# Optimization experiments

Measured on AMD Instinct MI355X. Metric: run time of the kernel, lower is better.

Reference implementation:

```python
import math
import jax, jax.numpy as jnp
import numpy as np

B, L, H = 32, 1024, 128

def setup_inputs() -> dict:
    key = jax.random.key(0)
    k1, k2, k3, k4 = jax.random.split(key, 4)
    a = jax.random.normal(k1, (B, L, H), dtype=jnp.float32)
    b = jax.random.normal(k2, (B, L, H), dtype=jnp.float32)
    mask_a = jax.random.randint(k3, (B, L, 1), 0, 2, dtype=jnp.int32)
    mask_b = jax.random.randint(k4, (B, L, 1), 0, 2, dtype=jnp.int32)
    temperature = jnp.asarray(1.0 / math.sqrt(H), dtype=jnp.float32)
    return {"a": a, "b": b, "mask_a": mask_a, "mask_b": mask_b, "temperature": temperature}

def reference(a, b, mask_a, mask_b, temperature):
    # scores: [B, La, Lb]
    scores = jnp.einsum('bld,bmd->blm', a, b) * temperature
    # outer product of token validity masks -> pair mask [B, La, Lb]
    mask = jnp.einsum('blk,bmk->blm', mask_a.astype(jnp.float32), mask_b.astype(jnp.float32)) > 0
    scores = jnp.where(mask, scores, jnp.float32(-10000.0))
    attention_a = jax.nn.softmax(scores, axis=1)  # normalize over La (columns)
    attention_b = jax.nn.softmax(scores, axis=2)  # normalize over Lb (rows)
    feature_a = jnp.einsum('blm,bmd->bld', attention_b, b)
    feature_b = jnp.einsum('blm,bmd->bld', attention_a, a)  # valid since La == Lb
    return (feature_a, feature_b)
```

## Files before the change

kernel.cpp:

```cpp
#include <hip/hip_runtime.h>
#include <math.h>

#define BN 32
#define LL 1024
#define HH 128

typedef __attribute__((ext_vector_type(8))) short short8;
typedef __attribute__((ext_vector_type(4))) float f32x4;

static const size_t SZ_BF = (size_t)BN * LL * HH * 2;

__device__ __forceinline__ ushort f2bf(float x) {
  union { float f; unsigned u; } c; c.f = x;
  unsigned r = c.u + 0x7fffu + ((c.u >> 16) & 1u);
  return (ushort)(r >> 16);
}
__device__ __forceinline__ float bf2f(ushort h) {
  union { unsigned u; float f; } c; c.u = ((unsigned)h) << 16;
  return c.f;
}
__device__ __forceinline__ short8 ld8(const ushort* p) {
  return *(const short8*)p;
}

__device__ __forceinline__ size_t chunkS(int bb, int g, int k) {
  return (((size_t)bb * 64 + g) * 4 + k) * 512;
}
__device__ __forceinline__ size_t chunkT(int bb, int dg, int mb) {
  return (((size_t)bb * 8 + dg) * 32 + mb) * 512;
}

__global__ __launch_bounds__(256) void k_convert(
    const float* __restrict__ a, const float* __restrict__ b,
    const int* __restrict__ mask_b,
    ushort* __restrict__ abfs, ushort* __restrict__ bbfs,
    ushort* __restrict__ aTs, ushort* __restrict__ bTs,
    float* __restrict__ meanb, float* __restrict__ invmean) {
  int bb = blockIdx.y;
  int l0 = blockIdx.x * 64;
  int which = blockIdx.z;
  const float* src = which ? b : a;
  ushort* dstS = which ? bbfs : abfs;
  ushort* dstT = which ? bTs : aTs;
  float* dmean = which ? meanb : invmean;
  __shared__ __align__(16) ushort T[128][72];
  __shared__ float accS[128];
  __shared__ float wgt[64];
  int t = threadIdx.x;
  if (t < 128) accS[t] = 0.f;
  if (t < 64)
    wgt[t] = which ? 1.0f : ((mask_b[bb * LL + l0 + t] == 0) ? 1.0f : 0.0f);
  int lrow = t >> 5;
  int dcol = (t & 31) * 4;
#pragma unroll
  for (int p = 0; p < 8; ++p) {
    int l = p * 8 + lrow;
    float4 v = *(const float4*)&src[((size_t)bb * LL + l0 + l) * HH + dcol];
    ushort4 u;
    u.x = f2bf(v.x); u.y = f2bf(v.y); u.z = f2bf(v.z); u.w = f2bf(v.w);
    int g = (l0 >> 4) + (l >> 4);
    int k = dcol >> 5, quadc = (dcol >> 3) & 3, j = dcol & 7;
    *(ushort4*)&dstS[chunkS(bb, g, k) + (size_t)(quadc * 16 + (l & 15)) * 8 + j] = u;
    T[dcol + 0][l] = u.x; T[dcol + 1][l] = u.y;
    T[dcol + 2][l] = u.z; T[dcol + 3][l] = u.w;
  }
  __syncthreads();
#pragma unroll
  for (int c = 0; c < 4; ++c) {
    int cid = c * 4 + (t >> 6);
    int dg = cid >> 1, mloc = cid & 1;
    int lane = t & 63, l16c = lane & 15, qc = lane >> 4;
    int row = dg * 16 + l16c, colb = mloc * 32 + qc * 8;
    uint2 vlo = *(const uint2*)&T[row][colb];
    uint2 vhi = *(const uint2*)&T[row][colb + 4];
    union { uint4 u4; short8 s8; ushort us[8]; } cv_;
    cv_.u4 = make_uint4(vlo.x, vlo.y, vhi.x, vhi.y);
    *(short8*)&dstT[chunkT(bb, dg, (l0 >> 5) + mloc) + (size_t)lane * 8] = cv_.s8;
    float s = 0.f;
#pragma unroll
    for (int jj = 0; jj < 8; ++jj) s += wgt[colb + jj] * bf2f(cv_.us[jj]);
    atomicAdd(&accS[row], s);
  }
  __syncthreads();
  if (t < 128) atomicAdd(&dmean[bb * HH + t], accS[t]);
}


__global__ __launch_bounds__(256, 2) void k_colsum(
    const ushort* __restrict__ abfs, const ushort* __restrict__ bbfs,
    ushort* __restrict__ aTm,
    const int* __restrict__ mask_a, const int* __restrict__ mask_b,
    const float* __restrict__ temp_p, float2* __restrict__ cc) {
  int wg = blockIdx.x;
  int xcd = wg & 7, k_ = wg >> 3;
  int bb = (k_ >> 4) * 8 + xcd;
  int m0 = (k_ & 15) * 64;
  int t = threadIdx.x;
  int w = t >> 6, lane = t & 63, l16 = lane & 15, quad = lane >> 4;
  float temp = temp_p[0];
  __shared__ __align__(16) float biasA[LL];
  __shared__ float csred[4][4][16];
  __shared__ float invS[64];
  for (int i = t; i < LL; i += 256)
    biasA[i] = mask_a[bb * LL + i] ? 0.0f : -10000.0f;

  short8 Bm[4][4];
  float biasB_mt[4];
#pragma unroll
  for (int mt = 0; mt < 4; ++mt) {
    int m = m0 + mt * 16 + l16;
    biasB_mt[mt] = mask_b[bb * LL + m] ? 0.0f : -10000.0f;
#pragma unroll
    for (int k = 0; k < 4; ++k)
      Bm[mt][k] = ld8(&bbfs[chunkS(bb, (m0 >> 4) + mt, k) + (size_t)lane * 8]);
  }
  __syncthreads();

  float cs[4] = {0.f, 0.f, 0.f, 0.f};
  short8 Al0[4], Al1[4];

#define LOADAL(AlX, IT)                                                       \
  {                                                                           \
    _Pragma("unroll") for (int k = 0; k < 4; ++k)                             \
        AlX[k] = ld8(&abfs[chunkS(bb, w * 16 + (IT), k) + (size_t)lane * 8]); \
  }

#define CSCOMPUTE(AlX, IT)                                                    \
  {                                                                           \
    int lbase = w * 256 + (IT) * 16;                                          \
    f32x4 bA = *(const f32x4*)&biasA[lbase + quad * 4];                       \
    _Pragma("unroll") for (int mt = 0; mt < 4; ++mt) {                        \
      f32x4 sacc = {0.f, 0.f, 0.f, 0.f};                                      \
      _Pragma("unroll") for (int k = 0; k < 4; ++k)                           \
          sacc = __builtin_amdgcn_mfma_f32_16x16x32_bf16(AlX[k], Bm[mt][k],   \
                                                         sacc, 0, 0, 0);      \
      _Pragma("unroll") for (int r = 0; r < 4; ++r)                           \
          cs[mt] += __expf(sacc[r] * temp + bA[r] + biasB_mt[mt]);            \
    }                                                                         \
  }

  LOADAL(Al0, 0);
  for (int it = 0; it < 16; it += 2) {
    LOADAL(Al1, it + 1);
    CSCOMPUTE(Al0, it);
    LOADAL(Al0, (it + 2) & 15);
    CSCOMPUTE(Al1, it + 1);
  }
#undef LOADAL
#undef CSCOMPUTE

#pragma unroll
  for (int mt = 0; mt < 4; ++mt) {
    cs[mt] += __shfl_xor(cs[mt], 16);
    cs[mt] += __shfl_xor(cs[mt], 32);
  }
  if (lane < 16) {
#pragma unroll
    for (int mt = 0; mt < 4; ++mt) csred[w][mt][l16] = cs[mt];
  }
  __syncthreads();
  if (t < 64) {
    int mt = t >> 4, ml = t & 15;
    float s = csred[0][mt][ml] + csred[1][mt][ml] + csred[2][mt][ml] + csred[3][mt][ml];
    int m = m0 + t;
    float bB = mask_b[bb * LL + m] ? 0.0f : -10000.0f;
    float inv = s > 0.f ? 1.0f / s : 0.0f;
    invS[t] = inv;
    cc[bb * LL + m] = make_float2(inv, bB);
  }
  __syncthreads();

#pragma unroll
  for (int q = 0; q < 4; ++q) {
    int cid = q * 4 + (t >> 6);
    int dg = cid >> 1, mloc = cid & 1;
    int ln = t & 63;
    ushort* ap = &aTm[chunkT(bb, dg, (m0 >> 5) + mloc) + (size_t)ln * 8];
    short8 v = ld8(ap);
    int mb = mloc * 32 + (ln >> 4) * 8;
    ushort o[8];
#pragma unroll
    for (int j = 0; j < 8; ++j) o[j] = f2bf(bf2f((ushort)v[j]) * invS[mb + j]);
    *(short8*)ap = *(short8*)&o[0];
  }
}

__global__ __launch_bounds__(256, 2) void k_features(
    const ushort* __restrict__ abfs, const ushort* __restrict__ bbfs,
    const ushort* __restrict__ aTs, const ushort* __restrict__ bTs,
    const int* __restrict__ mask_a, const float* __restrict__ temp_p,
    const float2* __restrict__ cc, const float* __restrict__ meanb,
    const float* __restrict__ invmean, float* __restrict__ out) {
  int wg = blockIdx.x;
  int xcd = wg & 7, k_ = wg >> 3;
  int bb = (k_ >> 4) * 8 + xcd;
  int l0 = (k_ & 15) * 64;
  int t = threadIdx.x;
  int w = t >> 6, lane = t & 63, l16 = lane & 15, quad = lane >> 4;
  float temp = temp_p[0];

  __shared__ float2 ccs[LL];
  __shared__ __align__(16) ushort Pa[2][64 * 72];
  __shared__ float rspart[4][64];
  __shared__ float rsfin[64];

  for (int i = t; i < LL; i += 256) ccs[i] = cc[bb * LL + i];

  float biasA_lt[4];
  short8 Afix[4][4];
#pragma unroll
  for (int lt = 0; lt < 4; ++lt) {
    int l = l0 + lt * 16 + l16;
    biasA_lt[lt] = mask_a[bb * LL + l] ? 0.0f : -10000.0f;
#pragma unroll
    for (int k = 0; k < 4; ++k)
      Afix[lt][k] = ld8(&abfs[chunkS(bb, (l0 >> 4) + lt, k) + (size_t)lane * 8]);
  }

  f32x4 accA[4][2], accB[4][2];
  f32x4 zero = {0.f, 0.f, 0.f, 0.f};
#pragma unroll
  for (int lt = 0; lt < 4; ++lt)
#pragma unroll
    for (int dt = 0; dt < 2; ++dt) { accA[lt][dt] = zero; accB[lt][dt] = zero; }
  float rs_lt[4] = {0.f, 0.f, 0.f, 0.f};
  __syncthreads();

  short8 Am0[4], Am1[4];
  float cv0[4], cv1[4];
  short8 Bb0[2][2], Ba0[2][2], Bb1[2][2], Ba1[2][2];

#define LOADAM(AmX, cvX, M0)                                                  \
  {                                                                           \
    _Pragma("unroll") for (int k = 0; k < 4; ++k)                             \
        AmX[k] = ld8(&bbfs[chunkS(bb, ((M0) >> 4) + w, k) + (size_t)lane * 8]); \
    _Pragma("unroll") for (int r = 0; r < 4; ++r)                             \
        cvX[r] = ccs[(M0) + w * 16 + quad * 4 + r].y;                         \
  }

#define LOADBT(BbX, BaX, M0)                                                  \
  {                                                                           \
    _Pragma("unroll") for (int dt = 0; dt < 2; ++dt) {                        \
      _Pragma("unroll") for (int ks = 0; ks < 2; ++ks) {                      \
        size_t cb = chunkT(bb, w * 2 + dt, ((M0) >> 5) + ks) + (size_t)lane * 8; \
        BbX[dt][ks] = ld8(&bTs[cb]);                                          \
        BaX[dt][ks] = ld8(&aTs[cb]);                                          \
      }                                                                       \
    }                                                                         \
  }

#define SPHASE(AmX, cvX, PBUFI)                                               \
  {                                                                           \
    ushort* pa = &Pa[PBUFI][0];                                               \
    _Pragma("unroll") for (int lt = 0; lt < 4; ++lt) {                        \
      f32x4 sacc = zero;                                                      \
      _Pragma("unroll") for (int k = 0; k < 4; ++k)                           \
          sacc = __builtin_amdgcn_mfma_f32_16x16x32_bf16(AmX[k], Afix[lt][k], \
                                                         sacc, 0, 0, 0);      \
      ushort pav[4];                                                          \
      _Pragma("unroll") for (int r = 0; r < 4; ++r) {                         \
        float e = __expf(sacc[r] * temp + biasA_lt[lt] + cvX[r]);             \
        pav[r] = f2bf(e);                                                     \
        rs_lt[lt] += bf2f(pav[r]);                                            \
      }                                                                       \
      uint2 ka;                                                               \
      ka.x = (uint)pav[0] | ((uint)pav[1] << 16);                             \
      ka.y = (uint)pav[2] | ((uint)pav[3] << 16);                             \
      int pidx = (lt * 16 + l16) * 72 + w * 16 + quad * 4;                    \
      *(uint2*)&pa[pidx] = ka;                                                \
    }                                                                         \
  }

#define FPHASE(PBUFI, BbX, BaX)                                               \
  {                                                                           \
    const ushort* pa = &Pa[PBUFI][0];                                         \
    _Pragma("unroll") for (int lt = 0; lt < 4; ++lt) {                        \
      _Pragma("unroll") for (int ks = 0; ks < 2; ++ks) {                      \
        int ridx = (lt * 16 + l16) * 72 + ks * 32 + quad * 8;                 \
        short8 PaF = *(const short8*)&pa[ridx];                               \
        _Pragma("unroll") for (int dt = 0; dt < 2; ++dt) {                    \
          accA[lt][dt] = __builtin_amdgcn_mfma_f32_16x16x32_bf16(             \
              PaF, BbX[dt][ks], accA[lt][dt], 0, 0, 0);                       \
          accB[lt][dt] = __builtin_amdgcn_mfma_f32_16x16x32_bf16(             \
              PaF, BaX[dt][ks], accB[lt][dt], 0, 0, 0);                       \
        }                                                                     \
      }                                                                       \
    }                                                                         \
  }

  LOADAM(Am0, cv0, 0);
  LOADBT(Bb0, Ba0, 0);
  LOADAM(Am1, cv1, 64);
  SPHASE(Am0, cv0, 0);
  __syncthreads();

  for (int kk = 0; kk < 7; ++kk) {
    int mA = (2 * kk + 1) * 64;
    LOADBT(Bb1, Ba1, mA);
    LOADAM(Am0, cv0, mA + 64);
    SPHASE(Am1, cv1, 1);
    FPHASE(0, Bb0, Ba0);
    __syncthreads();
    LOADBT(Bb0, Ba0, mA + 64);
    LOADAM(Am1, cv1, mA + 128);
    SPHASE(Am0, cv0, 0);
    FPHASE(1, Bb1, Ba1);
    __syncthreads();
  }

  LOADBT(Bb1, Ba1, 960);
  SPHASE(Am1, cv1, 1);
  FPHASE(0, Bb0, Ba0);
  __syncthreads();
  FPHASE(1, Bb1, Ba1);

#undef LOADAM
#undef LOADBT
#undef SPHASE
#undef FPHASE

#pragma unroll
  for (int lt = 0; lt < 4; ++lt) {
    rs_lt[lt] += __shfl_xor(rs_lt[lt], 16);
    rs_lt[lt] += __shfl_xor(rs_lt[lt], 32);
  }
  if (lane < 16) {
#pragma unroll
    for (int lt = 0; lt < 4; ++lt) rspart[w][lt * 16 + l16] = rs_lt[lt];
  }
  __syncthreads();
  if (t < 64)
    rsfin[t] = rspart[0][t] + rspart[1][t] + rspart[2][t] + rspart[3][t];
  __syncthreads();

  float* outA = out;
  float* outB = out + (size_t)BN * LL * HH;
#pragma unroll
  for (int dt = 0; dt < 2; ++dt) {
    int d = w * 32 + dt * 16 + l16;
    float mb = meanb[bb * HH + d] * (1.0f / 1024.0f);
    float im = invmean[bb * HH + d] * (1.0f / 1024.0f);
#pragma unroll
    for (int lt = 0; lt < 4; ++lt) {
#pragma unroll
      for (int r = 0; r < 4; ++r) {
        int l = lt * 16 + quad * 4 + r;
        float rsv = rsfin[l];
        float fa = (rsv > 0.f) ? accA[lt][dt][r] / rsv : mb;
        float fb = accB[lt][dt][r] + im;
        __builtin_nontemporal_store(fa, &outA[((size_t)bb * LL + l0 + l) * HH + d]);
        __builtin_nontemporal_store(fb, &outB[((size_t)bb * LL + l0 + l) * HH + d]);
      }
    }
  }
}

extern "C" void kernel_launch(void* const* d_in, const int* in_sizes, int n_in,
                              void* d_out, int out_size, void* d_ws, size_t ws_size,
                              hipStream_t stream) {
  const float* a = (const float*)d_in[0];
  const float* b = (const float*)d_in[1];
  const int* mask_a = (const int*)d_in[2];
  const int* mask_b = (const int*)d_in[3];
  const float* temp = (const float*)d_in[4];
  float* out = (float*)d_out;

  char* wsb = (char*)d_ws;
  ushort* abfs = (ushort*)(wsb + 0 * SZ_BF);
  ushort* bbfs = (ushort*)(wsb + 1 * SZ_BF);
  ushort* aTs  = (ushort*)(wsb + 2 * SZ_BF);
  ushort* bTs  = (ushort*)(wsb + 3 * SZ_BF);
  float2* cc  = (float2*)(wsb + 4 * SZ_BF);
  float* meanb   = (float*)(wsb + 4 * SZ_BF + (size_t)BN * LL * sizeof(float2));
  float* invmean = meanb + BN * HH;

  hipMemsetAsync(meanb, 0, 2 * BN * HH * sizeof(float), stream);
  k_convert<<<dim3(16, 32, 2), 256, 0, stream>>>(a, b, mask_b, abfs, bbfs, aTs,
                                                 bTs, meanb, invmean);
  k_colsum<<<dim3(512), 256, 0, stream>>>(abfs, bbfs, aTs, mask_a, mask_b, temp, cc);
  k_features<<<dim3(512), 256, 0, stream>>>(abfs, bbfs, aTs, bTs, mask_a, temp,
                                            cc, meanb, invmean, out);
  (void)in_sizes; (void)n_in; (void)out_size; (void)ws_size;
}
```

Before: 167.8 us.

## Materialize exponentiated scores in colsum pass and reuse them in feature GEMM

The column-sum kernel now writes the bf16 exponentiated masked scores to a workspace buffer in a tiled layout. A new feature kernel reads that buffer instead of recomputing the score GEMM and exponentials, and gets the row sums via an MFMA against a ones vector. This removes the duplicated QK^T and exp work but adds a large write and read of the score matrix through memory. The new path only runs when the workspace is large enough; otherwise the old kernels are used.

```diff
diff --git a/kernel.cpp b/kernel.cpp
--- a/kernel.cpp
+++ b/kernel.cpp
@@ -28,6 +28,9 @@
 }
 __device__ __forceinline__ size_t chunkT(int bb, int dg, int mb) {
   return (((size_t)bb * 8 + dg) * 32 + mb) * 512;
+}
+__device__ __forceinline__ size_t chunkE(int bb, int lg, int mk) {
+  return (((size_t)bb * 64 + lg) * 32 + mk) * 512;
 }
 
 __global__ __launch_bounds__(256) void k_convert(
@@ -185,6 +188,196 @@
   }
 }
 
+__global__ __launch_bounds__(256, 2) void k_colsum_e(
+    const ushort* __restrict__ abfs, const ushort* __restrict__ bbfs,
+    ushort* __restrict__ aTm, const int* __restrict__ mask_a,
+    const int* __restrict__ mask_b, const float* __restrict__ temp_p,
+    float2* __restrict__ cc, ushort* __restrict__ Ebuf) {
+  int wg = blockIdx.x;
+  int xcd = wg & 7, k_ = wg >> 3;
+  int bb = (k_ >> 4) * 8 + xcd;
+  int m0 = (k_ & 15) * 64;
+  int t = threadIdx.x;
+  int w = t >> 6, lane = t & 63, l16 = lane & 15, quad = lane >> 4;
+  float temp = temp_p[0];
+  __shared__ __align__(16) float biasA[LL];
+  __shared__ float csred[4][4][16];
+  __shared__ float invS[64];
+  __shared__ __align__(16) ushort Et[4][16][72];
+  for (int i = t; i < LL; i += 256)
+    biasA[i] = mask_a[bb * LL + i] ? 0.0f : -10000.0f;
+
+  short8 Bm[4][4];
+  float biasB_mt[4];
+#pragma unroll
+  for (int mt = 0; mt < 4; ++mt) {
+    int m = m0 + mt * 16 + l16;
+    biasB_mt[mt] = mask_b[bb * LL + m] ? 0.0f : -10000.0f;
+#pragma unroll
+    for (int k = 0; k < 4; ++k)
+      Bm[mt][k] = ld8(&bbfs[chunkS(bb, (m0 >> 4) + mt, k) + (size_t)lane * 8]);
+  }
+  __syncthreads();
+
+  float cs[4] = {0.f, 0.f, 0.f, 0.f};
+  short8 Al0[4], Al1[4];
+
+#define LOADAL(AlX, IT)                                                       \
+  {                                                                           \
+    _Pragma("unroll") for (int k = 0; k < 4; ++k)                             \
+        AlX[k] = ld8(&abfs[chunkS(bb, w * 16 + (IT), k) + (size_t)lane * 8]); \
+  }
+
+#define CSCOMPUTE_E(AlX, IT)                                                  \
+  {                                                                           \
+    f32x4 bA = *(const f32x4*)&biasA[w * 256 + (IT) * 16 + quad * 4];         \
+    _Pragma("unroll") for (int mt = 0; mt < 4; ++mt) {                        \
+      f32x4 sacc = {0.f, 0.f, 0.f, 0.f};                                      \
+      _Pragma("unroll") for (int k = 0; k < 4; ++k)                           \
+          sacc = __builtin_amdgcn_mfma_f32_16x16x32_bf16(AlX[k], Bm[mt][k],   \
+                                                         sacc, 0, 0, 0);      \
+      _Pragma("unroll") for (int r = 0; r < 4; ++r) {                         \
+        float e = __expf(sacc[r] * temp + bA[r] + biasB_mt[mt]);              \
+        cs[mt] += e;                                                          \
+        Et[w][quad * 4 + r][mt * 16 + l16] = f2bf(e);     \
+      }                                                                       \
+    }                                                                         \
+        \
+    _Pragma("unroll") for (int ks = 0; ks < 2; ++ks) {                        \
+      short8 ef = *(const short8*)&Et[w][l16][ks * 32 + quad * 8];            \
+      *(short8*)&Ebuf[chunkE(bb, w * 16 + (IT), (m0 >> 5) + ks) +             \
+                      (size_t)lane * 8] = ef;                                 \
+    }                                                                         \
+  }
+
+  LOADAL(Al0, 0);
+  for (int it = 0; it < 16; it += 2) {
+    LOADAL(Al1, it + 1);
+    CSCOMPUTE_E(Al0, it);
+    LOADAL(Al0, (it + 2) & 15);
+    CSCOMPUTE_E(Al1, it + 1);
+  }
+#undef LOADAL
+#undef CSCOMPUTE_E
+
+#pragma unroll
+  for (int mt = 0; mt < 4; ++mt) {
+    cs[mt] += __shfl_xor(cs[mt], 16);
+    cs[mt] += __shfl_xor(cs[mt], 32);
+  }
+  if (lane < 16) {
+#pragma unroll
+    for (int mt = 0; mt < 4; ++mt) csred[w][mt][l16] = cs[mt];
+  }
+  __syncthreads();
+  if (t < 64) {
+    int mt = t >> 4, ml = t & 15;
+    float s = csred[0][mt][ml] + csred[1][mt][ml] + csred[2][mt][ml] + csred[3][mt][ml];
+    int m = m0 + t;
+    float bB = mask_b[bb * LL + m] ? 0.0f : -10000.0f;
+    float inv = s > 0.f ? 1.0f / s : 0.0f;
+    invS[t] = inv;
+    cc[bb * LL + m] = make_float2(inv, bB);
+  }
+  __syncthreads();
+
+#pragma unroll
+  for (int q = 0; q < 4; ++q) {
+    int cid = q * 4 + (t >> 6);
+    int dg = cid >> 1, mloc = cid & 1;
+    int ln = t & 63;
+    ushort* ap = &aTm[chunkT(bb, dg, (m0 >> 5) + mloc) + (size_t)ln * 8];
+    short8 v = ld8(ap);
+    int mb = mloc * 32 + (ln >> 4) * 8;
+    ushort o[8];
+#pragma unroll
+    for (int j = 0; j < 8; ++j) o[j] = f2bf(bf2f((ushort)v[j]) * invS[mb + j]);
+    *(short8*)ap = *(short8*)&o[0];
+  }
+}
+
+__global__ __launch_bounds__(256, 2) void k_fgemm(
+    const ushort* __restrict__ aTs, const ushort* __restrict__ bTs,
+    const ushort* __restrict__ Ebuf, const float* __restrict__ meanb,
+    const float* __restrict__ invmean, float* __restrict__ out) {
+  int wg = blockIdx.x;
+  int xcd = wg & 7, k_ = wg >> 3;
+  int bb = (k_ >> 4) * 8 + xcd;
+  int l0 = (k_ & 15) * 64;
+  int t = threadIdx.x;
+  int w = t >> 6, lane = t & 63, l16 = lane & 15, quad = lane >> 4;
+
+  f32x4 accA[4][2], accB[4][2], accR[4];
+  f32x4 zero = {0.f, 0.f, 0.f, 0.f};
+#pragma unroll
+  for (int lt = 0; lt < 4; ++lt) {
+    accR[lt] = zero;
+#pragma unroll
+    for (int dt = 0; dt < 2; ++dt) { accA[lt][dt] = zero; accB[lt][dt] = zero; }
+  }
+  short8 ones;
+#pragma unroll
+  for (int j = 0; j < 8; ++j) ones[j] = (short)0x3F80;
+
+  short8 Ef0[4], Ef1[4], Tb0[2], Tb1[2], Ta0[2], Ta1[2];
+
+#define LOADOP(EfX, TbX, TaX, MS)                                             \
+  {                                                                           \
+    _Pragma("unroll") for (int lt = 0; lt < 4; ++lt)                          \
+        EfX[lt] = ld8(&Ebuf[chunkE(bb, (l0 >> 4) + lt, (MS)) + (size_t)lane * 8]); \
+    _Pragma("unroll") for (int dt = 0; dt < 2; ++dt) {                        \
+      size_t cb = chunkT(bb, w * 2 + dt, (MS)) + (size_t)lane * 8;            \
+      TbX[dt] = ld8(&bTs[cb]);                                                \
+      TaX[dt] = ld8(&aTs[cb]);                                                \
+    }                                                                         \
+  }
+
+#define FMAOP(EfX, TbX, TaX)                                                  \
+  {                                                                           \
+    _Pragma("unroll") for (int lt = 0; lt < 4; ++lt) {                        \
+      accR[lt] = __builtin_amdgcn_mfma_f32_16x16x32_bf16(ones, EfX[lt],       \
+                                                         accR[lt], 0, 0, 0); \
+      _Pragma("unroll") for (int dt = 0; dt < 2; ++dt) {                      \
+        accA[lt][dt] = __builtin_amdgcn_mfma_f32_16x16x32_bf16(               \
+            TbX[dt], EfX[lt], accA[lt][dt], 0, 0, 0);                         \
+        accB[lt][dt] = __builtin_amdgcn_mfma_f32_16x16x32_bf16(               \
+            TaX[dt], EfX[lt], accB[lt][dt], 0, 0, 0);                         \
+      }                                                                       \
+    }                                                                         \
+  }
+
+  LOADOP(Ef0, Tb0, Ta0, 0);
+  for (int ms = 0; ms < 32; ms += 2) {
+    LOADOP(Ef1, Tb1, Ta1, ms + 1);
+    FMAOP(Ef0, Tb0, Ta0);
+    LOADOP(Ef0, Tb0, Ta0, (ms + 2) & 31);
+    FMAOP(Ef1, Tb1, Ta1);
+  }
+#undef LOADOP
+#undef FMAOP
+
+  float* outA = out;
+  float* outB = out + (size_t)BN * LL * HH;
+#pragma unroll
+  for (int dt = 0; dt < 2; ++dt) {
+#pragma unroll
+    for (int r = 0; r < 4; ++r) {
+      int d = w * 32 + dt * 16 + quad * 4 + r;
+      float mb = meanb[bb * HH + d] * (1.0f / 1024.0f);
+      float im = invmean[bb * HH + d] * (1.0f / 1024.0f);
+#pragma unroll
+      for (int lt = 0; lt < 4; ++lt) {
+        int l = l0 + lt * 16 + l16;
+        float rsv = accR[lt][r];
+        float fa = (rsv > 0.f) ? accA[lt][dt][r] / rsv : mb;
+        float fb = accB[lt][dt][r] + im;
+        __builtin_nontemporal_store(fa, &outA[((size_t)bb * LL + l) * HH + d]);
+        __builtin_nontemporal_store(fb, &outB[((size_t)bb * LL + l) * HH + d]);
+      }
+    }
+  }
+}
+
 __global__ __launch_bounds__(256, 2) void k_features(
     const ushort* __restrict__ abfs, const ushort* __restrict__ bbfs,
     const ushort* __restrict__ aTs, const ushort* __restrict__ bTs,
@@ -373,12 +566,25 @@
   float2* cc  = (float2*)(wsb + 4 * SZ_BF);
   float* meanb   = (float*)(wsb + 4 * SZ_BF + (size_t)BN * LL * sizeof(float2));
   float* invmean = meanb + BN * HH;
+  size_t e_off = 4 * SZ_BF + (size_t)BN * LL * sizeof(float2) +
+                 2 * (size_t)BN * HH * sizeof(float);
+  e_off = (e_off + 1023) & ~(size_t)1023;
+  ushort* Ebuf = (ushort*)(wsb + e_off);
+  size_t need = e_off + (size_t)BN * LL * LL * 2;
+  bool use_e = (ws_size >= need);
 
   hipMemsetAsync(meanb, 0, 2 * BN * HH * sizeof(float), stream);
   k_convert<<<dim3(16, 32, 2), 256, 0, stream>>>(a, b, mask_b, abfs, bbfs, aTs,
                                                  bTs, meanb, invmean);
-  k_colsum<<<dim3(512), 256, 0, stream>>>(abfs, bbfs, aTs, mask_a, mask_b, temp, cc);
-  k_features<<<dim3(512), 256, 0, stream>>>(abfs, bbfs, aTs, bTs, mask_a, temp,
-                                            cc, meanb, invmean, out);
-  (void)in_sizes; (void)n_in; (void)out_size; (void)ws_size;
-}
+  if (use_e) {
+    k_colsum_e<<<dim3(512), 256, 0, stream>>>(abfs, bbfs, aTs, mask_a, mask_b,
+                                              temp, cc, Ebuf);
+    k_fgemm<<<dim3(512), 256, 0, stream>>>(aTs, bTs, Ebuf, meanb, invmean, out);
+  } else {
+    k_colsum<<<dim3(512), 256, 0, stream>>>(abfs, bbfs, aTs, mask_a, mask_b,
+                                            temp, cc);
+    k_features<<<dim3(512), 256, 0, stream>>>(abfs, bbfs, aTs, bTs, mask_a,
+                                              temp, cc, meanb, invmean, out);
+  }
+  (void)in_sizes; (void)n_in; (void)out_size;
+}
```

Result: slower. 210.8 us (+25.7%).
